# Performance work log

Hardware: AMD Instinct MI355X
Metric: run time of the kernel (lower is better)

The kernel has to match this reference:

```python
import jax, jax.numpy as jnp
import numpy as np

N_NODES = 50000
N_EDGES = 800000
DIM = 128
LN_EPS = 1e-5


def setup_inputs() -> dict:
    key = jax.random.key(0)
    k1, k2, k3, k4, k5 = jax.random.split(key, 5)
    x = jax.random.normal(k1, (N_NODES, DIM), dtype=jnp.float32)
    edge_index = jax.random.randint(k2, (2, N_EDGES), 0, N_NODES, dtype=jnp.int64)
    edge_weight = jax.random.uniform(k3, (N_EDGES,), dtype=jnp.float32)
    # GCNConv linear (PyG Linear: out = x @ W.T + b)
    W = jax.random.normal(k4, (DIM, DIM), dtype=jnp.float32) / np.sqrt(DIM)
    b = jnp.zeros((DIM,), dtype=jnp.float32)
    # pygnn.LayerNorm(dim, mode='node') affine params
    ln_weight = jnp.ones((DIM,), dtype=jnp.float32)
    ln_bias = jnp.zeros((DIM,), dtype=jnp.float32)
    return {"x": x, "edge_index": edge_index, "edge_weight": edge_weight,
            "W": W, "b": b, "ln_weight": ln_weight, "ln_bias": ln_bias}


def reference(x, edge_index, edge_weight, W, b, ln_weight, ln_bias):
    n = x.shape[0]
    # --- LayerNorm (mode='node'): per-node over feature dim ---
    mu = jnp.mean(x, axis=-1, keepdims=True)
    var = jnp.mean(jnp.square(x - mu), axis=-1, keepdims=True)
    xn = (x - mu) * jax.lax.rsqrt(var + LN_EPS) * ln_weight + ln_bias
    # --- GCNConv: linear first, then normalized propagate ---
    h = xn @ W.T  # [N, dim]
    row, col = edge_index[0], edge_index[1]  # source, target
    # add self loops (fill_value = 1.0)
    loop = jnp.arange(n, dtype=edge_index.dtype)
    row_f = jnp.concatenate([row, loop])
    col_f = jnp.concatenate([col, loop])
    ew_f = jnp.concatenate([edge_weight, jnp.ones((n,), dtype=edge_weight.dtype)])
    # symmetric gcn normalization: deg over target (col)
    deg = jax.ops.segment_sum(ew_f, col_f, num_segments=n)
    dinv = jnp.where(deg > 0, jax.lax.rsqrt(deg), 0.0)
    norm = dinv[row_f] * ew_f * dinv[col_f]  # [E+N]
    # gather-scale-scatter
    msg = h[row_f] * norm[:, None]  # [E+N, dim]
    out = jax.ops.segment_sum(msg, col_f, num_segments=n) + b
    # --- GELU (torch default = exact erf form); dropout is identity (p=0 / eval) ---
    return jax.nn.gelu(out, approximate=False)
```

## Files before the change

kernel.cpp:

```cpp
#include <hip/hip_runtime.h>
#include <math.h>

#define DIM 128
#define LN_EPS 1e-5f
#define HB 256
#define NSEG 8

typedef __attribute__((ext_vector_type(8))) short short8;
typedef __attribute__((ext_vector_type(4))) float floatx4;

__device__ __forceinline__ float gelu_exact(float v) {
    return 0.5f * v * (1.0f + erff(v * 0.70710678118654752f));
}
__device__ __forceinline__ float bf2f(unsigned short u) {
    return __uint_as_float(((unsigned)u) << 16);
}
__device__ __forceinline__ short f2bf(float f) {
    unsigned b = __float_as_uint(f);
    return (short)((b + 0x7FFF + ((b >> 16) & 1)) >> 16);
}

__global__ __launch_bounds__(256) void gemm_hist_kernel(
    const float* __restrict__ x, const float* __restrict__ W,
    const float* __restrict__ lnw, const float* __restrict__ lnb,
    unsigned short* __restrict__ h16,
    const int* __restrict__ col, int* __restrict__ hist,
    int n, int E, int nbkt)
{
    __shared__ short swb[2048 * 8];
    __shared__ short axb[1024 * 8];
    const int tid = threadIdx.x;

    if ((int)blockIdx.x < HB) {
        int* lh = (int*)swb;
        for (int b = tid; b < nbkt; b += 256) lh[b] = 0;
        __syncthreads();
        int g = blockIdx.x;
        int chunk = (E + HB - 1) / HB;
        int e0 = g * chunk;
        int e1 = e0 + chunk; if (e1 > E) e1 = E;
        for (int e = e0 + tid; e < e1; e += 256)
            atomicAdd(&lh[col[e] >> 6], 1);
        __syncthreads();
        for (int b = tid; b < nbkt; b += 256)
            hist[(size_t)g * nbkt + b] = lh[b];
        return;
    }

    const int gb = blockIdx.x - HB;
    const int n0 = gb * 64;

    for (int c = tid; c < 2048; c += 256) {
        int nrow = ((c >> 8) << 4) | (c & 15);
        int kb   = (((c >> 6) & 3) << 5) + (((c >> 4) & 3) << 3);
        const float* wp = W + nrow * DIM + kb;
        float4 w0 = *(const float4*)wp;
        float4 w1 = *(const float4*)(wp + 4);
        short8 p;
        p[0] = f2bf(w0.x); p[1] = f2bf(w0.y); p[2] = f2bf(w0.z); p[3] = f2bf(w0.w);
        p[4] = f2bf(w1.x); p[5] = f2bf(w1.y); p[6] = f2bf(w1.z); p[7] = f2bf(w1.w);
        *(short8*)&swb[c * 8] = p;
    }

    {
        int m = tid >> 2, sub = tid & 3;
        int node = n0 + m;
        bool valid = (node < n);
        const float4* xp = (const float4*)(x + (size_t)node * DIM + sub * 32);
        float4 v[8];
        float s = 0.f, ss = 0.f;
        #pragma unroll
        for (int i = 0; i < 8; ++i) {
            v[i] = valid ? xp[i] : make_float4(0.f, 0.f, 0.f, 0.f);
            s  += v[i].x + v[i].y + v[i].z + v[i].w;
            ss += v[i].x * v[i].x + v[i].y * v[i].y + v[i].z * v[i].z + v[i].w * v[i].w;
        }
        s += __shfl_xor(s, 1); ss += __shfl_xor(ss, 1);
        s += __shfl_xor(s, 2); ss += __shfl_xor(ss, 2);
        float mu   = s * (1.0f / 128.0f);
        float var  = ss * (1.0f / 128.0f) - mu * mu;
        float rstd = rsqrtf(var + LN_EPS);

        int mt = m >> 4, mloc = m & 15;
        #pragma unroll
        for (int quad = 0; quad < 4; ++quad) {
            float4 a = v[2 * quad], c4 = v[2 * quad + 1];
            const float4* lw = (const float4*)(lnw + sub * 32 + quad * 8);
            const float4* lb = (const float4*)(lnb + sub * 32 + quad * 8);
            float4 lw0 = lw[0], lw1 = lw[1], lb0 = lb[0], lb1 = lb[1];
            short8 p;
            p[0] = f2bf((a.x  - mu) * rstd * lw0.x + lb0.x);
            p[1] = f2bf((a.y  - mu) * rstd * lw0.y + lb0.y);
            p[2] = f2bf((a.z  - mu) * rstd * lw0.z + lb0.z);
            p[3] = f2bf((a.w  - mu) * rstd * lw0.w + lb0.w);
            p[4] = f2bf((c4.x - mu) * rstd * lw1.x + lb1.x);
            p[5] = f2bf((c4.y - mu) * rstd * lw1.y + lb1.y);
            p[6] = f2bf((c4.z - mu) * rstd * lw1.z + lb1.z);
            p[7] = f2bf((c4.w - mu) * rstd * lw1.w + lb1.w);
            int slot = mt * 256 + sub * 64 + quad * 16 + mloc;
            *(short8*)&axb[slot * 8] = p;
        }
    }
    __syncthreads();

    const int w    = tid >> 6;
    const int lane = tid & 63;

    short8 afrag[4];
    #pragma unroll
    for (int kq = 0; kq < 4; ++kq)
        afrag[kq] = *(const short8*)&axb[(w * 256 + kq * 64 + lane) * 8];

    floatx4 acc[8];
    #pragma unroll
    for (int jt = 0; jt < 8; ++jt) acc[jt] = (floatx4){0.f, 0.f, 0.f, 0.f};

    #pragma unroll
    for (int jt = 0; jt < 8; ++jt) {
        #pragma unroll
        for (int kq = 0; kq < 4; ++kq) {
            short8 bfrag = *(const short8*)&swb[(jt * 256 + kq * 64 + lane) * 8];
            acc[jt] = __builtin_amdgcn_mfma_f32_16x16x32_bf16(afrag[kq], bfrag,
                                                              acc[jt], 0, 0, 0);
        }
    }

    const int quad = lane >> 4, nl = lane & 15;
    #pragma unroll
    for (int jt = 0; jt < 8; ++jt) {
        #pragma unroll
        for (int r = 0; r < 4; ++r) {
            int rnode = n0 + w * 16 + quad * 4 + r;
            if (rnode < n)
                h16[(size_t)rnode * DIM + jt * 16 + nl] = (unsigned short)f2bf(acc[jt][r]);
        }
    }
}

__global__ __launch_bounds__(256) void seg_sum_kernel(
    const int* __restrict__ hist, int* __restrict__ segpart, int nbkt, int nq)
{
    int s = blockIdx.x / nq;
    int q = blockIdx.x % nq;
    int b = q * 256 + threadIdx.x;
    if (b >= nbkt) return;
    const int* hp = hist + (size_t)(s * (HB / NSEG)) * nbkt + b;
    int sum = 0;
    #pragma unroll 4
    for (int g = 0; g < HB / NSEG; ++g)
        sum += hp[(size_t)g * nbkt];
    segpart[(size_t)s * nbkt + b] = sum;
}

__global__ __launch_bounds__(256) void expand_kernel(
    const int* __restrict__ hist, const int* __restrict__ segpart,
    int* __restrict__ base, int* __restrict__ bktbase,
    int E, int nbkt, int nq)
{
    __shared__ int ls[256];
    const int tid = threadIdx.x;
    const int s = blockIdx.x / nq;
    const int q = blockIdx.x % nq;

    int excl_mine = 0;
    int carry = 0;
    for (int qq = 0; qq < nq; ++qq) {
        int b = qq * 256 + tid;
        int v = 0;
        if (b < nbkt) {
            #pragma unroll
            for (int ss = 0; ss < NSEG; ++ss)
                v += segpart[(size_t)ss * nbkt + b];
        }
        __syncthreads();
        ls[tid] = v;
        __syncthreads();
        int inc = v;
        for (int off = 1; off < 256; off <<= 1) {
            int add = (tid >= off) ? ls[tid - off] : 0;
            __syncthreads();
            inc += add;
            ls[tid] = inc;
            __syncthreads();
        }
        int ex = carry + inc - v;
        if (qq == q) excl_mine = ex;
        if (s == 0 && qq == q && b < nbkt) bktbase[b] = ex;
        carry += ls[255];
    }
    if (s == 0 && q == 0 && tid == 0) bktbase[nbkt] = E;

    int b = q * 256 + tid;
    if (b >= nbkt) return;
    int run = excl_mine;
    #pragma unroll
    for (int ss = 0; ss < NSEG; ++ss)
        if (ss < s) run += segpart[(size_t)ss * nbkt + b];
    int g0 = s * (HB / NSEG);
    for (int g = 0; g < HB / NSEG; ++g) {
        size_t idx = (size_t)(g0 + g) * nbkt + b;
        base[idx] = run;
        run += hist[idx];
    }
}

__global__ __launch_bounds__(256) void bucket_scatter_kernel(
    const int* __restrict__ row, const int* __restrict__ col,
    const float* __restrict__ ew, const int* __restrict__ base,
    int2* __restrict__ srt, int E, int nbkt)
{
    __shared__ int cur[1024];
    const int tid = threadIdx.x, g = blockIdx.x;
    for (int b = tid; b < nbkt; b += 256)
        cur[b] = base[(size_t)g * nbkt + b];
    __syncthreads();
    int chunk = (E + HB - 1) / HB;
    int e0 = g * chunk;
    int e1 = e0 + chunk; if (e1 > E) e1 = E;
    for (int e = e0 + tid; e < e1; e += 256) {
        int c = col[e];
        int pos = atomicAdd(&cur[c >> 6], 1);
        srt[pos] = make_int2(((c & 63) << 16) | row[e], __float_as_int(ew[e]));
    }
}

__global__ __launch_bounds__(256) void csr_kernel(
    const int2* __restrict__ srt, const int* __restrict__ bktbase,
    int2* __restrict__ edge_s, int* __restrict__ offsets,
    float* __restrict__ dinv, int n, int E)
{
    __shared__ int   k64[64];
    __shared__ float w64[64];
    __shared__ int   off64[64];
    __shared__ int   cur64[64];
    const int tid = threadIdx.x, b = blockIdx.x;
    if (tid < 64) { k64[tid] = 0; w64[tid] = 0.f; }
    __syncthreads();
    int s0 = bktbase[b], s1 = bktbase[b + 1];
    for (int i = s0 + tid; i < s1; i += 256) {
        int2 v = srt[i];
        int d = (v.x >> 16) & 63;
        atomicAdd(&k64[d], 1);
        atomicAdd(&w64[d], __int_as_float(v.y));
    }
    __syncthreads();
    if (tid == 0) {
        int run = 0;
        #pragma unroll
        for (int d = 0; d < 64; ++d) { off64[d] = run; cur64[d] = run; run += k64[d]; }
    }
    __syncthreads();
    if (tid < 64) {
        int dest = b * 64 + tid;
        if (dest < n) {
            offsets[dest] = s0 + off64[tid];
            dinv[dest]    = rsqrtf(1.0f + w64[tid]);
        }
    }
    if (b == 0 && tid == 0) offsets[n] = E;
    for (int i = s0 + tid; i < s1; i += 256) {
        int2 v = srt[i];
        int d = (v.x >> 16) & 63;
        int p = atomicAdd(&cur64[d], 1);
        edge_s[s0 + p] = make_int2(v.x & 0xFFFF, v.y);
    }
}

__global__ __launch_bounds__(256) void gather4_kernel(
    const int* __restrict__ offsets, const int2* __restrict__ edge_s,
    const float* __restrict__ dinv, const unsigned short* __restrict__ h16,
    const float* __restrict__ bias, float* __restrict__ out, int n)
{
    int wave = (blockIdx.x * 256 + threadIdx.x) >> 6;
    int lane = threadIdx.x & 63;
    int grp  = lane >> 4;
    int sub  = lane & 15;
    int node = wave * 4 + grp;
    if (node >= n) return;

    int beg = offsets[node], end = offsets[node + 1];
    float di = dinv[node];
    short8 sv = *(const short8*)(h16 + (size_t)node * DIM + sub * 8);
    float s2 = di * di;
    float acc[8];
    #pragma unroll
    for (int d = 0; d < 8; ++d) acc[d] = s2 * bf2f((unsigned short)sv[d]);

    int j = beg;
    for (; j + 3 < end; j += 4) {
        int2 e0 = edge_s[j],     e1 = edge_s[j + 1];
        int2 e2 = edge_s[j + 2], e3 = edge_s[j + 3];
        short8 a0 = *(const short8*)(h16 + (size_t)e0.x * DIM + sub * 8);
        short8 a1 = *(const short8*)(h16 + (size_t)e1.x * DIM + sub * 8);
        short8 a2 = *(const short8*)(h16 + (size_t)e2.x * DIM + sub * 8);
        short8 a3 = *(const short8*)(h16 + (size_t)e3.x * DIM + sub * 8);
        float n0 = dinv[e0.x] * __int_as_float(e0.y) * di;
        float n1 = dinv[e1.x] * __int_as_float(e1.y) * di;
        float n2 = dinv[e2.x] * __int_as_float(e2.y) * di;
        float n3 = dinv[e3.x] * __int_as_float(e3.y) * di;
        #pragma unroll
        for (int d = 0; d < 8; ++d) {
            acc[d] = fmaf(n0, bf2f((unsigned short)a0[d]), acc[d]);
            acc[d] = fmaf(n1, bf2f((unsigned short)a1[d]), acc[d]);
            acc[d] = fmaf(n2, bf2f((unsigned short)a2[d]), acc[d]);
            acc[d] = fmaf(n3, bf2f((unsigned short)a3[d]), acc[d]);
        }
    }
    for (; j < end; ++j) {
        int2 e0 = edge_s[j];
        float n0 = dinv[e0.x] * __int_as_float(e0.y) * di;
        short8 a = *(const short8*)(h16 + (size_t)e0.x * DIM + sub * 8);
        #pragma unroll
        for (int d = 0; d < 8; ++d) acc[d] = fmaf(n0, bf2f((unsigned short)a[d]), acc[d]);
    }

    float4 b0 = *(const float4*)(bias + sub * 8);
    float4 b1 = *(const float4*)(bias + sub * 8 + 4);
    float4 o0, o1;
    o0.x = gelu_exact(acc[0] + b0.x); o0.y = gelu_exact(acc[1] + b0.y);
    o0.z = gelu_exact(acc[2] + b0.z); o0.w = gelu_exact(acc[3] + b0.w);
    o1.x = gelu_exact(acc[4] + b1.x); o1.y = gelu_exact(acc[5] + b1.y);
    o1.z = gelu_exact(acc[6] + b1.z); o1.w = gelu_exact(acc[7] + b1.w);
    float* op = out + (size_t)node * DIM + sub * 8;
    *(float4*)op       = o0;
    *(float4*)(op + 4) = o1;
}

extern "C" void kernel_launch(void* const* d_in, const int* in_sizes, int n_in,
                              void* d_out, int out_size, void* d_ws, size_t ws_size,
                              hipStream_t stream)
{
    const float* x    = (const float*)d_in[0];
    const int*   ei   = (const int*)d_in[1];
    const float* ew   = (const float*)d_in[2];
    const float* W    = (const float*)d_in[3];
    const float* b    = (const float*)d_in[4];
    const float* ln_w = (const float*)d_in[5];
    const float* ln_b = (const float*)d_in[6];
    float* out = (float*)d_out;

    const int n = in_sizes[0] / DIM;
    const int E = in_sizes[2];
    const int* row  = ei;
    const int* colp = ei + E;
    const int nbkt = (n + 63) / 64;
    const int nq   = (nbkt + 255) / 256;

    int2*           srt     = (int2*)d_ws;
    int2*           edge_s  = srt + E;
    unsigned short* h16     = (unsigned short*)(edge_s + E);
    int*            hist    = (int*)(h16 + (size_t)n * DIM);
    int*            base    = hist + (size_t)HB * nbkt;
    int*            segpart = base + (size_t)HB * nbkt;
    int*            bktbase = segpart + (size_t)NSEG * nbkt;
    int*            offsets = bktbase + nbkt + 1;
    float*          dinv    = (float*)(offsets + n + 1);

    const int GB = (n + 63) / 64;

    gemm_hist_kernel<<<HB + GB, 256, 0, stream>>>(x, W, ln_w, ln_b, h16,
                                                  colp, hist, n, E, nbkt);
    seg_sum_kernel<<<NSEG * nq, 256, 0, stream>>>(hist, segpart, nbkt, nq);
    expand_kernel<<<NSEG * nq, 256, 0, stream>>>(hist, segpart, base, bktbase,
                                                 E, nbkt, nq);
    bucket_scatter_kernel<<<HB, 256, 0, stream>>>(row, colp, ew, base, srt, E, nbkt);
    csr_kernel<<<nbkt, 256, 0, stream>>>(srt, bktbase, edge_s, offsets, dinv, n, E);
    {
        int waves  = (n + 3) / 4;
        int blocks = (waves + 3) / 4;
        gather4_kernel<<<blocks, 256, 0, stream>>>(offsets, edge_s, dinv, h16, b, out, n);
    }
}
```

Baseline: 177.1 us.

## Replace two-level bucket sort CSR build with global-atomic degree count and direct scatter

The multi-stage bucket histogram, segment-sum, expand, bucket-scatter and per-bucket CSR passes are replaced. The new path counts per-node degree and weight sum with global float atomics, scans the counts into offsets, and scatters edges straight to their final CSR slots with global atomics on a per-node cursor. The full edge norm is now precomputed during the scatter, so the gather loop no longer loads dinv per edge. This cuts kernel count and the intermediate sort buffer, at the cost of heavily contended global atomics, non-deterministic edge order within each node, and a fixed 256-block scan limit (nblk must be ≤256, which holds for 50k nodes).

```diff
diff --git a/kernel.cpp b/kernel.cpp
--- a/kernel.cpp
+++ b/kernel.cpp
@@ -4,7 +4,6 @@
 #define DIM 128
 #define LN_EPS 1e-5f
 #define HB 256
-#define NSEG 8
 
 typedef __attribute__((ext_vector_type(8))) short short8;
 typedef __attribute__((ext_vector_type(4))) float floatx4;
@@ -20,30 +19,35 @@
     return (short)((b + 0x7FFF + ((b >> 16) & 1)) >> 16);
 }
 
-__global__ __launch_bounds__(256) void gemm_hist_kernel(
+__global__ __launch_bounds__(256) void zero_kernel(float2* __restrict__ deg, int n)
+{
+    int i = blockIdx.x * 256 + threadIdx.x;
+    if (i < n) deg[i] = make_float2(0.f, 0.f);
+}
+
+__global__ __launch_bounds__(256) void gemm_deg_kernel(
     const float* __restrict__ x, const float* __restrict__ W,
     const float* __restrict__ lnw, const float* __restrict__ lnb,
     unsigned short* __restrict__ h16,
-    const int* __restrict__ col, int* __restrict__ hist,
-    int n, int E, int nbkt)
+    const int* __restrict__ col, const float* __restrict__ ew,
+    float2* __restrict__ deg,
+    int n, int E)
 {
     __shared__ short swb[2048 * 8];
     __shared__ short axb[1024 * 8];
     const int tid = threadIdx.x;
 
     if ((int)blockIdx.x < HB) {
-        int* lh = (int*)swb;
-        for (int b = tid; b < nbkt; b += 256) lh[b] = 0;
-        __syncthreads();
         int g = blockIdx.x;
         int chunk = (E + HB - 1) / HB;
         int e0 = g * chunk;
         int e1 = e0 + chunk; if (e1 > E) e1 = E;
-        for (int e = e0 + tid; e < e1; e += 256)
-            atomicAdd(&lh[col[e] >> 6], 1);
-        __syncthreads();
-        for (int b = tid; b < nbkt; b += 256)
-            hist[(size_t)g * nbkt + b] = lh[b];
+        for (int e = e0 + tid; e < e1; e += 256) {
+            int c = col[e];
+            float w = ew[e];
+            atomicAdd(&deg[c].x, 1.0f);
+            atomicAdd(&deg[c].y, w);
+        }
         return;
     }
 
@@ -137,133 +141,82 @@
     }
 }
 
-__global__ __launch_bounds__(256) void seg_sum_kernel(
-    const int* __restrict__ hist, int* __restrict__ segpart, int nbkt, int nq)
-{
-    int s = blockIdx.x / nq;
-    int q = blockIdx.x % nq;
-    int b = q * 256 + threadIdx.x;
-    if (b >= nbkt) return;
-    const int* hp = hist + (size_t)(s * (HB / NSEG)) * nbkt + b;
-    int sum = 0;
-    #pragma unroll 4
-    for (int g = 0; g < HB / NSEG; ++g)
-        sum += hp[(size_t)g * nbkt];
-    segpart[(size_t)s * nbkt + b] = sum;
-}
-
-__global__ __launch_bounds__(256) void expand_kernel(
-    const int* __restrict__ hist, const int* __restrict__ segpart,
-    int* __restrict__ base, int* __restrict__ bktbase,
-    int E, int nbkt, int nq)
+__global__ __launch_bounds__(256) void part_kernel(
+    const float2* __restrict__ deg, int* __restrict__ part,
+    float* __restrict__ dinv, int n)
+{
+    __shared__ int ws[4];
+    const int tid = threadIdx.x;
+    int i = blockIdx.x * 256 + tid;
+    int c = 0;
+    if (i < n) {
+        float2 d = deg[i];
+        c = (int)d.x;
+        dinv[i] = rsqrtf(1.0f + d.y);
+    }
+    int cs = c;
+    cs += __shfl_xor(cs, 1);  cs += __shfl_xor(cs, 2);  cs += __shfl_xor(cs, 4);
+    cs += __shfl_xor(cs, 8);  cs += __shfl_xor(cs, 16); cs += __shfl_xor(cs, 32);
+    if ((tid & 63) == 0) ws[tid >> 6] = cs;
+    __syncthreads();
+    if (tid == 0) part[blockIdx.x] = ws[0] + ws[1] + ws[2] + ws[3];
+}
+
+__global__ __launch_bounds__(256) void scan_kernel(
+    const float2* __restrict__ deg, const int* __restrict__ part,
+    int* __restrict__ offsets, int* __restrict__ cursor,
+    int nblk, int n, int E)
 {
     __shared__ int ls[256];
+    __shared__ int spref;
     const int tid = threadIdx.x;
-    const int s = blockIdx.x / nq;
-    const int q = blockIdx.x % nq;
-
-    int excl_mine = 0;
-    int carry = 0;
-    for (int qq = 0; qq < nq; ++qq) {
-        int b = qq * 256 + tid;
-        int v = 0;
-        if (b < nbkt) {
-            #pragma unroll
-            for (int ss = 0; ss < NSEG; ++ss)
-                v += segpart[(size_t)ss * nbkt + b];
-        }
+
+    int v = (tid < nblk) ? part[tid] : 0;
+    ls[tid] = v;
+    __syncthreads();
+    int inc = v;
+    for (int off = 1; off < 256; off <<= 1) {
+        int add = (tid >= off) ? ls[tid - off] : 0;
         __syncthreads();
-        ls[tid] = v;
+        inc += add;
+        ls[tid] = inc;
         __syncthreads();
-        int inc = v;
-        for (int off = 1; off < 256; off <<= 1) {
-            int add = (tid >= off) ? ls[tid - off] : 0;
-            __syncthreads();
-            inc += add;
-            ls[tid] = inc;
-            __syncthreads();
-        }
-        int ex = carry + inc - v;
-        if (qq == q) excl_mine = ex;
-        if (s == 0 && qq == q && b < nbkt) bktbase[b] = ex;
-        carry += ls[255];
-    }
-    if (s == 0 && q == 0 && tid == 0) bktbase[nbkt] = E;
-
-    int b = q * 256 + tid;
-    if (b >= nbkt) return;
-    int run = excl_mine;
-    #pragma unroll
-    for (int ss = 0; ss < NSEG; ++ss)
-        if (ss < s) run += segpart[(size_t)ss * nbkt + b];
-    int g0 = s * (HB / NSEG);
-    for (int g = 0; g < HB / NSEG; ++g) {
-        size_t idx = (size_t)(g0 + g) * nbkt + b;
-        base[idx] = run;
-        run += hist[idx];
-    }
-}
-
-__global__ __launch_bounds__(256) void bucket_scatter_kernel(
+    }
+    if (tid == (int)blockIdx.x) spref = inc - v;
+    __syncthreads();
+    const int P = spref;
+
+    int i = blockIdx.x * 256 + tid;
+    int c = (i < n) ? (int)deg[i].x : 0;
+    ls[tid] = c;
+    __syncthreads();
+    int inc2 = c;
+    for (int off = 1; off < 256; off <<= 1) {
+        int add = (tid >= off) ? ls[tid - off] : 0;
+        __syncthreads();
+        inc2 += add;
+        ls[tid] = inc2;
+        __syncthreads();
+    }
+    if (i < n) {
+        int ex = P + inc2 - c;
+        offsets[i] = ex;
+        cursor[i]  = ex;
+    }
+    if (blockIdx.x == 0 && tid == 0) offsets[n] = E;
+}
+
+__global__ __launch_bounds__(256) void scatter_kernel(
     const int* __restrict__ row, const int* __restrict__ col,
-    const float* __restrict__ ew, const int* __restrict__ base,
-    int2* __restrict__ srt, int E, int nbkt)
-{
-    __shared__ int cur[1024];
-    const int tid = threadIdx.x, g = blockIdx.x;
-    for (int b = tid; b < nbkt; b += 256)
-        cur[b] = base[(size_t)g * nbkt + b];
-    __syncthreads();
-    int chunk = (E + HB - 1) / HB;
-    int e0 = g * chunk;
-    int e1 = e0 + chunk; if (e1 > E) e1 = E;
-    for (int e = e0 + tid; e < e1; e += 256) {
-        int c = col[e];
-        int pos = atomicAdd(&cur[c >> 6], 1);
-        srt[pos] = make_int2(((c & 63) << 16) | row[e], __float_as_int(ew[e]));
-    }
-}
-
-__global__ __launch_bounds__(256) void csr_kernel(
-    const int2* __restrict__ srt, const int* __restrict__ bktbase,
-    int2* __restrict__ edge_s, int* __restrict__ offsets,
-    float* __restrict__ dinv, int n, int E)
-{
-    __shared__ int   k64[64];
-    __shared__ float w64[64];
-    __shared__ int   off64[64];
-    __shared__ int   cur64[64];
-    const int tid = threadIdx.x, b = blockIdx.x;
-    if (tid < 64) { k64[tid] = 0; w64[tid] = 0.f; }
-    __syncthreads();
-    int s0 = bktbase[b], s1 = bktbase[b + 1];
-    for (int i = s0 + tid; i < s1; i += 256) {
-        int2 v = srt[i];
-        int d = (v.x >> 16) & 63;
-        atomicAdd(&k64[d], 1);
-        atomicAdd(&w64[d], __int_as_float(v.y));
-    }
-    __syncthreads();
-    if (tid == 0) {
-        int run = 0;
-        #pragma unroll
-        for (int d = 0; d < 64; ++d) { off64[d] = run; cur64[d] = run; run += k64[d]; }
-    }
-    __syncthreads();
-    if (tid < 64) {
-        int dest = b * 64 + tid;
-        if (dest < n) {
-            offsets[dest] = s0 + off64[tid];
-            dinv[dest]    = rsqrtf(1.0f + w64[tid]);
-        }
-    }
-    if (b == 0 && tid == 0) offsets[n] = E;
-    for (int i = s0 + tid; i < s1; i += 256) {
-        int2 v = srt[i];
-        int d = (v.x >> 16) & 63;
-        int p = atomicAdd(&cur64[d], 1);
-        edge_s[s0 + p] = make_int2(v.x & 0xFFFF, v.y);
-    }
+    const float* __restrict__ ew, const float* __restrict__ dinv,
+    int* __restrict__ cursor, int2* __restrict__ edge_s, int E)
+{
+    int e = blockIdx.x * 256 + threadIdx.x;
+    if (e >= E) return;
+    int r = row[e], c = col[e];
+    float nrm = dinv[r] * ew[e] * dinv[c];
+    int pos = atomicAdd(&cursor[c], 1);
+    edge_s[pos] = make_int2(r, __float_as_int(nrm));
 }
 
 __global__ __launch_bounds__(256) void gather4_kernel(
@@ -294,10 +247,10 @@
         short8 a1 = *(const short8*)(h16 + (size_t)e1.x * DIM + sub * 8);
         short8 a2 = *(const short8*)(h16 + (size_t)e2.x * DIM + sub * 8);
         short8 a3 = *(const short8*)(h16 + (size_t)e3.x * DIM + sub * 8);
-        float n0 = dinv[e0.x] * __int_as_float(e0.y) * di;
-        float n1 = dinv[e1.x] * __int_as_float(e1.y) * di;
-        float n2 = dinv[e2.x] * __int_as_float(e2.y) * di;
-        float n3 = dinv[e3.x] * __int_as_float(e3.y) * di;
+        float n0 = __int_as_float(e0.y);
+        float n1 = __int_as_float(e1.y);
+        float n2 = __int_as_float(e2.y);
+        float n3 = __int_as_float(e3.y);
         #pragma unroll
         for (int d = 0; d < 8; ++d) {
             acc[d] = fmaf(n0, bf2f((unsigned short)a0[d]), acc[d]);
@@ -308,7 +261,7 @@
     }
     for (; j < end; ++j) {
         int2 e0 = edge_s[j];
-        float n0 = dinv[e0.x] * __int_as_float(e0.y) * di;
+        float n0 = __int_as_float(e0.y);
         short8 a = *(const short8*)(h16 + (size_t)e0.x * DIM + sub * 8);
         #pragma unroll
         for (int d = 0; d < 8; ++d) acc[d] = fmaf(n0, bf2f((unsigned short)a[d]), acc[d]);
@@ -343,28 +296,25 @@
     const int E = in_sizes[2];
     const int* row  = ei;
     const int* colp = ei + E;
-    const int nbkt = (n + 63) / 64;
-    const int nq   = (nbkt + 255) / 256;
-
-    int2*           srt     = (int2*)d_ws;
-    int2*           edge_s  = srt + E;
+
+    int2*           edge_s  = (int2*)d_ws;
     unsigned short* h16     = (unsigned short*)(edge_s + E);
-    int*            hist    = (int*)(h16 + (size_t)n * DIM);
-    int*            base    = hist + (size_t)HB * nbkt;
-    int*            segpart = base + (size_t)HB * nbkt;
-    int*            bktbase = segpart + (size_t)NSEG * nbkt;
-    int*            offsets = bktbase + nbkt + 1;
+    float2*         deg     = (float2*)(h16 + (size_t)n * DIM);
+    int*            cursor  = (int*)(deg + n);
+    int*            offsets = cursor + n;
     float*          dinv    = (float*)(offsets + n + 1);
-
-    const int GB = (n + 63) / 64;
-
-    gemm_hist_kernel<<<HB + GB, 256, 0, stream>>>(x, W, ln_w, ln_b, h16,
-                                                  colp, hist, n, E, nbkt);
-    seg_sum_kernel<<<NSEG * nq, 256, 0, stream>>>(hist, segpart, nbkt, nq);
-    expand_kernel<<<NSEG * nq, 256, 0, stream>>>(hist, segpart, base, bktbase,
-                                                 E, nbkt, nq);
-    bucket_scatter_kernel<<<HB, 256, 0, stream>>>(row, colp, ew, base, srt, E, nbkt);
-    csr_kernel<<<nbkt, 256, 0, stream>>>(srt, bktbase, edge_s, offsets, dinv, n, E);
+    int*            part    = (int*)(dinv + n);
+
+    const int GB   = (n + 63) / 64;
+    const int nblk = (n + 255) / 256;
+
+    zero_kernel<<<nblk, 256, 0, stream>>>(deg, n);
+    gemm_deg_kernel<<<HB + GB, 256, 0, stream>>>(x, W, ln_w, ln_b, h16,
+                                                 colp, ew, deg, n, E);
+    part_kernel<<<nblk, 256, 0, stream>>>(deg, part, dinv, n);
+    scan_kernel<<<nblk, 256, 0, stream>>>(deg, part, offsets, cursor, nblk, n, E);
+    scatter_kernel<<<(E + 255) / 256, 256, 0, stream>>>(row, colp, ew, dinv,
+                                                        cursor, edge_s, E);
     {
         int waves  = (n + 3) / 4;
         int blocks = (waves + 3) / 4;
```

After: 259.9 us. 1.47x slower.

## Precompute bf16 W fragments once, restructure bucket prefix scan, fold target dinv into edges

Applied to the files above, without the earlier changes.

A separate small kernel now converts W to bf16 MFMA fragment layout once, and the GEMM blocks read B fragments straight from global memory (L2-cached) instead of each block converting W into shared memory. This removes redundant per-block conversion and LDS use, which may raise occupancy. The histogram prefix is now built per bucket: one block reduces each bucket's totals and another computes the bucket offsets and scans across the 256 histogram blocks, replacing the segmented two-pass scheme. The CSR kernel also multiplies the target dinv into the stored edge weight, so the gather loop skips that multiply.

```diff
diff --git a/kernel.cpp b/kernel.cpp
--- a/kernel.cpp
+++ b/kernel.cpp
@@ -4,7 +4,6 @@
 #define DIM 128
 #define LN_EPS 1e-5f
 #define HB 256
-#define NSEG 8
 
 typedef __attribute__((ext_vector_type(8))) short short8;
 typedef __attribute__((ext_vector_type(4))) float floatx4;
@@ -20,19 +19,33 @@
     return (short)((b + 0x7FFF + ((b >> 16) & 1)) >> 16);
 }
 
+__global__ __launch_bounds__(256) void wconv_kernel(
+    const float* __restrict__ W, short* __restrict__ wfrag)
+{
+    int c = blockIdx.x * 256 + threadIdx.x;
+    int nrow = ((c >> 8) << 4) | (c & 15);
+    int kb   = (((c >> 6) & 3) << 5) + (((c >> 4) & 3) << 3);
+    const float* wp = W + nrow * DIM + kb;
+    float4 w0 = *(const float4*)wp;
+    float4 w1 = *(const float4*)(wp + 4);
+    short8 p;
+    p[0] = f2bf(w0.x); p[1] = f2bf(w0.y); p[2] = f2bf(w0.z); p[3] = f2bf(w0.w);
+    p[4] = f2bf(w1.x); p[5] = f2bf(w1.y); p[6] = f2bf(w1.z); p[7] = f2bf(w1.w);
+    *(short8*)&wfrag[c * 8] = p;
+}
+
 __global__ __launch_bounds__(256) void gemm_hist_kernel(
-    const float* __restrict__ x, const float* __restrict__ W,
+    const float* __restrict__ x, const short* __restrict__ wfrag,
     const float* __restrict__ lnw, const float* __restrict__ lnb,
     unsigned short* __restrict__ h16,
     const int* __restrict__ col, int* __restrict__ hist,
     int n, int E, int nbkt)
 {
-    __shared__ short swb[2048 * 8];
     __shared__ short axb[1024 * 8];
     const int tid = threadIdx.x;
 
     if ((int)blockIdx.x < HB) {
-        int* lh = (int*)swb;
+        int* lh = (int*)axb;
         for (int b = tid; b < nbkt; b += 256) lh[b] = 0;
         __syncthreads();
         int g = blockIdx.x;
@@ -49,18 +62,6 @@
 
     const int gb = blockIdx.x - HB;
     const int n0 = gb * 64;
-
-    for (int c = tid; c < 2048; c += 256) {
-        int nrow = ((c >> 8) << 4) | (c & 15);
-        int kb   = (((c >> 6) & 3) << 5) + (((c >> 4) & 3) << 3);
-        const float* wp = W + nrow * DIM + kb;
-        float4 w0 = *(const float4*)wp;
-        float4 w1 = *(const float4*)(wp + 4);
-        short8 p;
-        p[0] = f2bf(w0.x); p[1] = f2bf(w0.y); p[2] = f2bf(w0.z); p[3] = f2bf(w0.w);
-        p[4] = f2bf(w1.x); p[5] = f2bf(w1.y); p[6] = f2bf(w1.z); p[7] = f2bf(w1.w);
-        *(short8*)&swb[c * 8] = p;
-    }
 
     {
         int m = tid >> 2, sub = tid & 3;
@@ -105,6 +106,7 @@
 
     const int w    = tid >> 6;
     const int lane = tid & 63;
+    const short8* wf = (const short8*)wfrag;
 
     short8 afrag[4];
     #pragma unroll
@@ -119,7 +121,7 @@
     for (int jt = 0; jt < 8; ++jt) {
         #pragma unroll
         for (int kq = 0; kq < 4; ++kq) {
-            short8 bfrag = *(const short8*)&swb[(jt * 256 + kq * 64 + lane) * 8];
+            short8 bfrag = wf[jt * 256 + kq * 64 + lane];
             acc[jt] = __builtin_amdgcn_mfma_f32_16x16x32_bf16(afrag[kq], bfrag,
                                                               acc[jt], 0, 0, 0);
         }
@@ -137,41 +139,34 @@
     }
 }
 
-__global__ __launch_bounds__(256) void seg_sum_kernel(
-    const int* __restrict__ hist, int* __restrict__ segpart, int nbkt, int nq)
-{
-    int s = blockIdx.x / nq;
-    int q = blockIdx.x % nq;
-    int b = q * 256 + threadIdx.x;
-    if (b >= nbkt) return;
-    const int* hp = hist + (size_t)(s * (HB / NSEG)) * nbkt + b;
-    int sum = 0;
-    #pragma unroll 4
-    for (int g = 0; g < HB / NSEG; ++g)
-        sum += hp[(size_t)g * nbkt];
-    segpart[(size_t)s * nbkt + b] = sum;
+__global__ __launch_bounds__(256) void tot_kernel(
+    const int* __restrict__ hist, int* __restrict__ tot, int nbkt)
+{
+    __shared__ int ws[4];
+    const int tid = threadIdx.x;
+    const int b = blockIdx.x;
+    int v = hist[(size_t)tid * nbkt + b];
+    v += __shfl_xor(v, 1);  v += __shfl_xor(v, 2);  v += __shfl_xor(v, 4);
+    v += __shfl_xor(v, 8);  v += __shfl_xor(v, 16); v += __shfl_xor(v, 32);
+    if ((tid & 63) == 0) ws[tid >> 6] = v;
+    __syncthreads();
+    if (tid == 0) tot[b] = ws[0] + ws[1] + ws[2] + ws[3];
 }
 
 __global__ __launch_bounds__(256) void expand_kernel(
-    const int* __restrict__ hist, const int* __restrict__ segpart,
-    int* __restrict__ base, int* __restrict__ bktbase,
-    int E, int nbkt, int nq)
+    const int* __restrict__ hist, const int* __restrict__ tot,
+    int* __restrict__ base, int* __restrict__ bktbase, int nbkt, int E)
 {
     __shared__ int ls[256];
+    __shared__ int sbb;
     const int tid = threadIdx.x;
-    const int s = blockIdx.x / nq;
-    const int q = blockIdx.x % nq;
-
-    int excl_mine = 0;
+    const int b = blockIdx.x;
+    const int nq = (nbkt + 255) / 256;
+
     int carry = 0;
     for (int qq = 0; qq < nq; ++qq) {
-        int b = qq * 256 + tid;
-        int v = 0;
-        if (b < nbkt) {
-            #pragma unroll
-            for (int ss = 0; ss < NSEG; ++ss)
-                v += segpart[(size_t)ss * nbkt + b];
-        }
+        int i = qq * 256 + tid;
+        int v = (i < nbkt) ? tot[i] : 0;
         __syncthreads();
         ls[tid] = v;
         __syncthreads();
@@ -183,25 +178,27 @@
             ls[tid] = inc;
             __syncthreads();
         }
-        int ex = carry + inc - v;
-        if (qq == q) excl_mine = ex;
-        if (s == 0 && qq == q && b < nbkt) bktbase[b] = ex;
+        if (i == b) sbb = carry + inc - v;
         carry += ls[255];
     }
-    if (s == 0 && q == 0 && tid == 0) bktbase[nbkt] = E;
-
-    int b = q * 256 + tid;
-    if (b >= nbkt) return;
-    int run = excl_mine;
-    #pragma unroll
-    for (int ss = 0; ss < NSEG; ++ss)
-        if (ss < s) run += segpart[(size_t)ss * nbkt + b];
-    int g0 = s * (HB / NSEG);
-    for (int g = 0; g < HB / NSEG; ++g) {
-        size_t idx = (size_t)(g0 + g) * nbkt + b;
-        base[idx] = run;
-        run += hist[idx];
-    }
+    __syncthreads();
+    const int bb = sbb;
+    if (tid == 0) bktbase[b] = bb;
+    if (b == 0 && tid == 0) bktbase[nbkt] = E;
+
+    int h = hist[(size_t)tid * nbkt + b];
+    __syncthreads();
+    ls[tid] = h;
+    __syncthreads();
+    int inc2 = h;
+    for (int off = 1; off < 256; off <<= 1) {
+        int add = (tid >= off) ? ls[tid - off] : 0;
+        __syncthreads();
+        inc2 += add;
+        ls[tid] = inc2;
+        __syncthreads();
+    }
+    base[(size_t)tid * nbkt + b] = bb + inc2 - h;
 }
 
 __global__ __launch_bounds__(256) void bucket_scatter_kernel(
@@ -231,6 +228,7 @@
 {
     __shared__ int   k64[64];
     __shared__ float w64[64];
+    __shared__ float di64[64];
     __shared__ int   off64[64];
     __shared__ int   cur64[64];
     const int tid = threadIdx.x, b = blockIdx.x;
@@ -252,17 +250,21 @@
     __syncthreads();
     if (tid < 64) {
         int dest = b * 64 + tid;
+        float dv = rsqrtf(1.0f + w64[tid]);
+        di64[tid] = dv;
         if (dest < n) {
             offsets[dest] = s0 + off64[tid];
-            dinv[dest]    = rsqrtf(1.0f + w64[tid]);
+            dinv[dest]    = dv;
         }
     }
     if (b == 0 && tid == 0) offsets[n] = E;
+    __syncthreads();
     for (int i = s0 + tid; i < s1; i += 256) {
         int2 v = srt[i];
         int d = (v.x >> 16) & 63;
         int p = atomicAdd(&cur64[d], 1);
-        edge_s[s0 + p] = make_int2(v.x & 0xFFFF, v.y);
+        edge_s[s0 + p] = make_int2(v.x & 0xFFFF,
+                                   __float_as_int(__int_as_float(v.y) * di64[d]));
     }
 }
 
@@ -294,10 +296,10 @@
         short8 a1 = *(const short8*)(h16 + (size_t)e1.x * DIM + sub * 8);
         short8 a2 = *(const short8*)(h16 + (size_t)e2.x * DIM + sub * 8);
         short8 a3 = *(const short8*)(h16 + (size_t)e3.x * DIM + sub * 8);
-        float n0 = dinv[e0.x] * __int_as_float(e0.y) * di;
-        float n1 = dinv[e1.x] * __int_as_float(e1.y) * di;
-        float n2 = dinv[e2.x] * __int_as_float(e2.y) * di;
-        float n3 = dinv[e3.x] * __int_as_float(e3.y) * di;
+        float n0 = dinv[e0.x] * __int_as_float(e0.y);
+        float n1 = dinv[e1.x] * __int_as_float(e1.y);
+        float n2 = dinv[e2.x] * __int_as_float(e2.y);
+        float n3 = dinv[e3.x] * __int_as_float(e3.y);
         #pragma unroll
         for (int d = 0; d < 8; ++d) {
             acc[d] = fmaf(n0, bf2f((unsigned short)a0[d]), acc[d]);
@@ -308,7 +310,7 @@
     }
     for (; j < end; ++j) {
         int2 e0 = edge_s[j];
-        float n0 = dinv[e0.x] * __int_as_float(e0.y) * di;
+        float n0 = dinv[e0.x] * __int_as_float(e0.y);
         short8 a = *(const short8*)(h16 + (size_t)e0.x * DIM + sub * 8);
         #pragma unroll
         for (int d = 0; d < 8; ++d) acc[d] = fmaf(n0, bf2f((unsigned short)a[d]), acc[d]);
@@ -344,25 +346,25 @@
     const int* row  = ei;
     const int* colp = ei + E;
     const int nbkt = (n + 63) / 64;
-    const int nq   = (nbkt + 255) / 256;
 
     int2*           srt     = (int2*)d_ws;
     int2*           edge_s  = srt + E;
     unsigned short* h16     = (unsigned short*)(edge_s + E);
-    int*            hist    = (int*)(h16 + (size_t)n * DIM);
+    short*          wfrag   = (short*)(h16 + (size_t)n * DIM);
+    int*            hist    = (int*)(wfrag + 16384);
     int*            base    = hist + (size_t)HB * nbkt;
-    int*            segpart = base + (size_t)HB * nbkt;
-    int*            bktbase = segpart + (size_t)NSEG * nbkt;
+    int*            tot     = base + (size_t)HB * nbkt;
+    int*            bktbase = tot + nbkt;
     int*            offsets = bktbase + nbkt + 1;
     float*          dinv    = (float*)(offsets + n + 1);
 
     const int GB = (n + 63) / 64;
 
-    gemm_hist_kernel<<<HB + GB, 256, 0, stream>>>(x, W, ln_w, ln_b, h16,
+    wconv_kernel<<<8, 256, 0, stream>>>(W, wfrag);
+    gemm_hist_kernel<<<HB + GB, 256, 0, stream>>>(x, wfrag, ln_w, ln_b, h16,
                                                   colp, hist, n, E, nbkt);
-    seg_sum_kernel<<<NSEG * nq, 256, 0, stream>>>(hist, segpart, nbkt, nq);
-    expand_kernel<<<NSEG * nq, 256, 0, stream>>>(hist, segpart, base, bktbase,
-                                                 E, nbkt, nq);
+    tot_kernel<<<nbkt, 256, 0, stream>>>(hist, tot, nbkt);
+    expand_kernel<<<nbkt, 256, 0, stream>>>(hist, tot, base, bktbase, nbkt, E);
     bucket_scatter_kernel<<<HB, 256, 0, stream>>>(row, colp, ew, base, srt, E, nbkt);
     csr_kernel<<<nbkt, 256, 0, stream>>>(srt, bktbase, edge_s, offsets, dinv, n, E);
     {
```

After: 178.5 us. No clear change (+0.8%).

## Replace global CSR build with fixed-capacity buckets and fuse per-bucket sort into gather

Applied to the files above, without the earlier changes.

Edges are now scattered into fixed-capacity (CAP) slots per 64-node bucket, which makes the global scan unnecessary and lets a one-block-per-bucket expand kernel replace the seg_sum and multi-pass expand kernels. The CSR kernel and edge_s buffer are removed. The gather kernel now loads each bucket's edges into LDS, counting-sorts them by destination, and precomputes the per-edge normalisation there before gathering. It also adds a slow fallback for buckets over capacity and doubles the histogram block count. The aim is to cut kernel launches and global round-trips. The cost is fewer, LDS-heavy gather blocks (about 32KB each), which lowers parallelism and occupancy.

```diff
diff --git a/kernel.cpp b/kernel.cpp
--- a/kernel.cpp
+++ b/kernel.cpp
@@ -3,8 +3,8 @@
 
 #define DIM 128
 #define LN_EPS 1e-5f
-#define HB 256
-#define NSEG 8
+#define HB 512
+#define CAP 2048
 
 typedef __attribute__((ext_vector_type(8))) short short8;
 typedef __attribute__((ext_vector_type(4))) float floatx4;
@@ -137,71 +137,32 @@
     }
 }
 
-__global__ __launch_bounds__(256) void seg_sum_kernel(
-    const int* __restrict__ hist, int* __restrict__ segpart, int nbkt, int nq)
-{
-    int s = blockIdx.x / nq;
-    int q = blockIdx.x % nq;
-    int b = q * 256 + threadIdx.x;
-    if (b >= nbkt) return;
-    const int* hp = hist + (size_t)(s * (HB / NSEG)) * nbkt + b;
-    int sum = 0;
-    #pragma unroll 4
-    for (int g = 0; g < HB / NSEG; ++g)
-        sum += hp[(size_t)g * nbkt];
-    segpart[(size_t)s * nbkt + b] = sum;
-}
-
 __global__ __launch_bounds__(256) void expand_kernel(
-    const int* __restrict__ hist, const int* __restrict__ segpart,
-    int* __restrict__ base, int* __restrict__ bktbase,
-    int E, int nbkt, int nq)
+    const int* __restrict__ hist, int* __restrict__ base,
+    int* __restrict__ cnt, int nbkt)
 {
     __shared__ int ls[256];
     const int tid = threadIdx.x;
-    const int s = blockIdx.x / nq;
-    const int q = blockIdx.x % nq;
-
-    int excl_mine = 0;
-    int carry = 0;
-    for (int qq = 0; qq < nq; ++qq) {
-        int b = qq * 256 + tid;
-        int v = 0;
-        if (b < nbkt) {
-            #pragma unroll
-            for (int ss = 0; ss < NSEG; ++ss)
-                v += segpart[(size_t)ss * nbkt + b];
-        }
-        __syncthreads();
-        ls[tid] = v;
-        __syncthreads();
-        int inc = v;
-        for (int off = 1; off < 256; off <<= 1) {
-            int add = (tid >= off) ? ls[tid - off] : 0;
-            __syncthreads();
-            inc += add;
-            ls[tid] = inc;
-            __syncthreads();
-        }
-        int ex = carry + inc - v;
-        if (qq == q) excl_mine = ex;
-        if (s == 0 && qq == q && b < nbkt) bktbase[b] = ex;
-        carry += ls[255];
-    }
-    if (s == 0 && q == 0 && tid == 0) bktbase[nbkt] = E;
-
-    int b = q * 256 + tid;
-    if (b >= nbkt) return;
-    int run = excl_mine;
-    #pragma unroll
-    for (int ss = 0; ss < NSEG; ++ss)
-        if (ss < s) run += segpart[(size_t)ss * nbkt + b];
-    int g0 = s * (HB / NSEG);
-    for (int g = 0; g < HB / NSEG; ++g) {
-        size_t idx = (size_t)(g0 + g) * nbkt + b;
-        base[idx] = run;
-        run += hist[idx];
-    }
+    const int b = blockIdx.x;
+
+    int v0 = hist[(size_t)(2 * tid)     * nbkt + b];
+    int v1 = hist[(size_t)(2 * tid + 1) * nbkt + b];
+    int p = v0 + v1;
+    ls[tid] = p;
+    __syncthreads();
+    int inc = p;
+    for (int off = 1; off < 256; off <<= 1) {
+        int add = (tid >= off) ? ls[tid - off] : 0;
+        __syncthreads();
+        inc += add;
+        ls[tid] = inc;
+        __syncthreads();
+    }
+    int ex = inc - p;
+    int a0 = b * CAP + ex;
+    base[(size_t)(2 * tid)     * nbkt + b] = a0;
+    base[(size_t)(2 * tid + 1) * nbkt + b] = a0 + v0;
+    if (tid == 255) cnt[b] = inc;
 }
 
 __global__ __launch_bounds__(256) void bucket_scatter_kernel(
@@ -224,106 +185,154 @@
     }
 }
 
-__global__ __launch_bounds__(256) void csr_kernel(
-    const int2* __restrict__ srt, const int* __restrict__ bktbase,
-    int2* __restrict__ edge_s, int* __restrict__ offsets,
-    float* __restrict__ dinv, int n, int E)
-{
-    __shared__ int   k64[64];
+__global__ __launch_bounds__(256) void dinv_kernel(
+    const int2* __restrict__ srt, const int* __restrict__ cnt,
+    float* __restrict__ dinv, int n)
+{
     __shared__ float w64[64];
-    __shared__ int   off64[64];
-    __shared__ int   cur64[64];
     const int tid = threadIdx.x, b = blockIdx.x;
-    if (tid < 64) { k64[tid] = 0; w64[tid] = 0.f; }
-    __syncthreads();
-    int s0 = bktbase[b], s1 = bktbase[b + 1];
-    for (int i = s0 + tid; i < s1; i += 256) {
-        int2 v = srt[i];
-        int d = (v.x >> 16) & 63;
-        atomicAdd(&k64[d], 1);
-        atomicAdd(&w64[d], __int_as_float(v.y));
-    }
-    __syncthreads();
-    if (tid == 0) {
-        int run = 0;
-        #pragma unroll
-        for (int d = 0; d < 64; ++d) { off64[d] = run; cur64[d] = run; run += k64[d]; }
-    }
-    __syncthreads();
-    if (tid < 64) {
-        int dest = b * 64 + tid;
-        if (dest < n) {
-            offsets[dest] = s0 + off64[tid];
-            dinv[dest]    = rsqrtf(1.0f + w64[tid]);
-        }
-    }
-    if (b == 0 && tid == 0) offsets[n] = E;
-    for (int i = s0 + tid; i < s1; i += 256) {
-        int2 v = srt[i];
-        int d = (v.x >> 16) & 63;
-        int p = atomicAdd(&cur64[d], 1);
-        edge_s[s0 + p] = make_int2(v.x & 0xFFFF, v.y);
-    }
-}
-
-__global__ __launch_bounds__(256) void gather4_kernel(
-    const int* __restrict__ offsets, const int2* __restrict__ edge_s,
+    if (tid < 64) w64[tid] = 0.f;
+    __syncthreads();
+    int c = cnt[b];
+    int s0 = b * CAP;
+    for (int i = tid; i < c; i += 256) {
+        int2 v = srt[s0 + i];
+        atomicAdd(&w64[(v.x >> 16) & 63], __int_as_float(v.y));
+    }
+    __syncthreads();
+    if (tid < 64)
+        dinv[b * 64 + tid] = rsqrtf(1.0f + w64[tid]);
+}
+
+__global__ __launch_bounds__(256) void bucket_gather_kernel(
+    const int2* __restrict__ srt, const int* __restrict__ cnt,
     const float* __restrict__ dinv, const unsigned short* __restrict__ h16,
     const float* __restrict__ bias, float* __restrict__ out, int n)
 {
-    int wave = (blockIdx.x * 256 + threadIdx.x) >> 6;
-    int lane = threadIdx.x & 63;
-    int grp  = lane >> 4;
-    int sub  = lane & 15;
-    int node = wave * 4 + grp;
-    if (node >= n) return;
-
-    int beg = offsets[node], end = offsets[node + 1];
-    float di = dinv[node];
-    short8 sv = *(const short8*)(h16 + (size_t)node * DIM + sub * 8);
-    float s2 = di * di;
-    float acc[8];
-    #pragma unroll
-    for (int d = 0; d < 8; ++d) acc[d] = s2 * bf2f((unsigned short)sv[d]);
-
-    int j = beg;
-    for (; j + 3 < end; j += 4) {
-        int2 e0 = edge_s[j],     e1 = edge_s[j + 1];
-        int2 e2 = edge_s[j + 2], e3 = edge_s[j + 3];
-        short8 a0 = *(const short8*)(h16 + (size_t)e0.x * DIM + sub * 8);
-        short8 a1 = *(const short8*)(h16 + (size_t)e1.x * DIM + sub * 8);
-        short8 a2 = *(const short8*)(h16 + (size_t)e2.x * DIM + sub * 8);
-        short8 a3 = *(const short8*)(h16 + (size_t)e3.x * DIM + sub * 8);
-        float n0 = dinv[e0.x] * __int_as_float(e0.y) * di;
-        float n1 = dinv[e1.x] * __int_as_float(e1.y) * di;
-        float n2 = dinv[e2.x] * __int_as_float(e2.y) * di;
-        float n3 = dinv[e3.x] * __int_as_float(e3.y) * di;
-        #pragma unroll
-        for (int d = 0; d < 8; ++d) {
-            acc[d] = fmaf(n0, bf2f((unsigned short)a0[d]), acc[d]);
-            acc[d] = fmaf(n1, bf2f((unsigned short)a1[d]), acc[d]);
-            acc[d] = fmaf(n2, bf2f((unsigned short)a2[d]), acc[d]);
-            acc[d] = fmaf(n3, bf2f((unsigned short)a3[d]), acc[d]);
-        }
-    }
-    for (; j < end; ++j) {
-        int2 e0 = edge_s[j];
-        float n0 = dinv[e0.x] * __int_as_float(e0.y) * di;
-        short8 a = *(const short8*)(h16 + (size_t)e0.x * DIM + sub * 8);
-        #pragma unroll
-        for (int d = 0; d < 8; ++d) acc[d] = fmaf(n0, bf2f((unsigned short)a[d]), acc[d]);
-    }
-
-    float4 b0 = *(const float4*)(bias + sub * 8);
-    float4 b1 = *(const float4*)(bias + sub * 8 + 4);
-    float4 o0, o1;
-    o0.x = gelu_exact(acc[0] + b0.x); o0.y = gelu_exact(acc[1] + b0.y);
-    o0.z = gelu_exact(acc[2] + b0.z); o0.w = gelu_exact(acc[3] + b0.w);
-    o1.x = gelu_exact(acc[4] + b1.x); o1.y = gelu_exact(acc[5] + b1.y);
-    o1.z = gelu_exact(acc[6] + b1.z); o1.w = gelu_exact(acc[7] + b1.w);
-    float* op = out + (size_t)node * DIM + sub * 8;
-    *(float4*)op       = o0;
-    *(float4*)(op + 4) = o1;
+    __shared__ int2  bufA[CAP];
+    __shared__ int2  bufB[CAP];
+    __shared__ int   k64[64], off64[64], cur64[64];
+    __shared__ float di64[64];
+    const int tid = threadIdx.x, b = blockIdx.x;
+
+    if (tid < 64) { k64[tid] = 0; di64[tid] = dinv[b * 64 + tid]; }
+    __syncthreads();
+
+    const int c  = cnt[b];
+    const int s0 = b * CAP;
+    const int grp = tid >> 4;
+    const int sub = tid & 15;
+
+    if (c <= CAP) {
+        for (int i = tid; i < c; i += 256) {
+            int2 v = srt[s0 + i];
+            bufA[i] = v;
+            atomicAdd(&k64[(v.x >> 16) & 63], 1);
+        }
+        __syncthreads();
+        if (tid == 0) {
+            int run = 0;
+            #pragma unroll
+            for (int d = 0; d < 64; ++d) { off64[d] = run; cur64[d] = run; run += k64[d]; }
+        }
+        __syncthreads();
+        for (int i = tid; i < c; i += 256) {
+            int2 v = bufA[i];
+            int d   = (v.x >> 16) & 63;
+            int src = v.x & 0xFFFF;
+            float nrm = dinv[src] * __int_as_float(v.y) * di64[d];
+            int p = atomicAdd(&cur64[d], 1);
+            bufB[p] = make_int2(src, __float_as_int(nrm));
+        }
+        __syncthreads();
+
+        #pragma unroll
+        for (int dd = 0; dd < 4; ++dd) {
+            int d = dd * 16 + grp;
+            int dest = b * 64 + d;
+            if (dest >= n) continue;
+            float di = di64[d];
+            short8 sv = *(const short8*)(h16 + (size_t)dest * DIM + sub * 8);
+            float s2 = di * di;
+            float acc[8];
+            #pragma unroll
+            for (int k = 0; k < 8; ++k) acc[k] = s2 * bf2f((unsigned short)sv[k]);
+
+            int j  = off64[d];
+            int je = j + k64[d];
+            for (; j + 3 < je; j += 4) {
+                int2 e0 = bufB[j],     e1 = bufB[j + 1];
+                int2 e2 = bufB[j + 2], e3 = bufB[j + 3];
+                short8 a0 = *(const short8*)(h16 + (size_t)e0.x * DIM + sub * 8);
+                short8 a1 = *(const short8*)(h16 + (size_t)e1.x * DIM + sub * 8);
+                short8 a2 = *(const short8*)(h16 + (size_t)e2.x * DIM + sub * 8);
+                short8 a3 = *(const short8*)(h16 + (size_t)e3.x * DIM + sub * 8);
+                float n0 = __int_as_float(e0.y);
+                float n1 = __int_as_float(e1.y);
+                float n2 = __int_as_float(e2.y);
+                float n3 = __int_as_float(e3.y);
+                #pragma unroll
+                for (int k = 0; k < 8; ++k) {
+                    acc[k] = fmaf(n0, bf2f((unsigned short)a0[k]), acc[k]);
+                    acc[k] = fmaf(n1, bf2f((unsigned short)a1[k]), acc[k]);
+                    acc[k] = fmaf(n2, bf2f((unsigned short)a2[k]), acc[k]);
+                    acc[k] = fmaf(n3, bf2f((unsigned short)a3[k]), acc[k]);
+                }
+            }
+            for (; j < je; ++j) {
+                int2 e0 = bufB[j];
+                float n0 = __int_as_float(e0.y);
+                short8 a = *(const short8*)(h16 + (size_t)e0.x * DIM + sub * 8);
+                #pragma unroll
+                for (int k = 0; k < 8; ++k)
+                    acc[k] = fmaf(n0, bf2f((unsigned short)a[k]), acc[k]);
+            }
+
+            float4 b0 = *(const float4*)(bias + sub * 8);
+            float4 b1 = *(const float4*)(bias + sub * 8 + 4);
+            float4 o0, o1;
+            o0.x = gelu_exact(acc[0] + b0.x); o0.y = gelu_exact(acc[1] + b0.y);
+            o0.z = gelu_exact(acc[2] + b0.z); o0.w = gelu_exact(acc[3] + b0.w);
+            o1.x = gelu_exact(acc[4] + b1.x); o1.y = gelu_exact(acc[5] + b1.y);
+            o1.z = gelu_exact(acc[6] + b1.z); o1.w = gelu_exact(acc[7] + b1.w);
+            float* op = out + (size_t)dest * DIM + sub * 8;
+            *(float4*)op       = o0;
+            *(float4*)(op + 4) = o1;
+        }
+    } else {
+        #pragma unroll
+        for (int dd = 0; dd < 4; ++dd) {
+            int d = dd * 16 + grp;
+            int dest = b * 64 + d;
+            if (dest >= n) continue;
+            float di = di64[d];
+            short8 sv = *(const short8*)(h16 + (size_t)dest * DIM + sub * 8);
+            float s2 = di * di;
+            float acc[8];
+            #pragma unroll
+            for (int k = 0; k < 8; ++k) acc[k] = s2 * bf2f((unsigned short)sv[k]);
+            for (int i = 0; i < c; ++i) {
+                int2 v = srt[s0 + i];
+                if (((v.x >> 16) & 63) != d) continue;
+                int src = v.x & 0xFFFF;
+                float nrm = dinv[src] * __int_as_float(v.y) * di;
+                short8 a = *(const short8*)(h16 + (size_t)src * DIM + sub * 8);
+                #pragma unroll
+                for (int k = 0; k < 8; ++k)
+                    acc[k] = fmaf(nrm, bf2f((unsigned short)a[k]), acc[k]);
+            }
+            float4 b0 = *(const float4*)(bias + sub * 8);
+            float4 b1 = *(const float4*)(bias + sub * 8 + 4);
+            float4 o0, o1;
+            o0.x = gelu_exact(acc[0] + b0.x); o0.y = gelu_exact(acc[1] + b0.y);
+            o0.z = gelu_exact(acc[2] + b0.z); o0.w = gelu_exact(acc[3] + b0.w);
+            o1.x = gelu_exact(acc[4] + b1.x); o1.y = gelu_exact(acc[5] + b1.y);
+            o1.z = gelu_exact(acc[6] + b1.z); o1.w = gelu_exact(acc[7] + b1.w);
+            float* op = out + (size_t)dest * DIM + sub * 8;
+            *(float4*)op       = o0;
+            *(float4*)(op + 4) = o1;
+        }
+    }
 }
 
 extern "C" void kernel_launch(void* const* d_in, const int* in_sizes, int n_in,
@@ -344,30 +353,20 @@
     const int* row  = ei;
     const int* colp = ei + E;
     const int nbkt = (n + 63) / 64;
-    const int nq   = (nbkt + 255) / 256;
-
-    int2*           srt     = (int2*)d_ws;
-    int2*           edge_s  = srt + E;
-    unsigned short* h16     = (unsigned short*)(edge_s + E);
-    int*            hist    = (int*)(h16 + (size_t)n * DIM);
-    int*            base    = hist + (size_t)HB * nbkt;
-    int*            segpart = base + (size_t)HB * nbkt;
-    int*            bktbase = segpart + (size_t)NSEG * nbkt;
-    int*            offsets = bktbase + nbkt + 1;
-    float*          dinv    = (float*)(offsets + n + 1);
+
+    int2*           srt  = (int2*)d_ws;
+    unsigned short* h16  = (unsigned short*)(srt + (size_t)nbkt * CAP);
+    int*            hist = (int*)(h16 + (size_t)n * DIM);
+    int*            base = hist + (size_t)HB * nbkt;
+    int*            cnt  = base + (size_t)HB * nbkt;
+    float*          dinv = (float*)(cnt + nbkt);
 
     const int GB = (n + 63) / 64;
 
     gemm_hist_kernel<<<HB + GB, 256, 0, stream>>>(x, W, ln_w, ln_b, h16,
                                                   colp, hist, n, E, nbkt);
-    seg_sum_kernel<<<NSEG * nq, 256, 0, stream>>>(hist, segpart, nbkt, nq);
-    expand_kernel<<<NSEG * nq, 256, 0, stream>>>(hist, segpart, base, bktbase,
-                                                 E, nbkt, nq);
+    expand_kernel<<<nbkt, 256, 0, stream>>>(hist, base, cnt, nbkt);
     bucket_scatter_kernel<<<HB, 256, 0, stream>>>(row, colp, ew, base, srt, E, nbkt);
-    csr_kernel<<<nbkt, 256, 0, stream>>>(srt, bktbase, edge_s, offsets, dinv, n, E);
-    {
-        int waves  = (n + 3) / 4;
-        int blocks = (waves + 3) / 4;
-        gather4_kernel<<<blocks, 256, 0, stream>>>(offsets, edge_s, dinv, h16, b, out, n);
-    }
-}
+    dinv_kernel<<<nbkt, 256, 0, stream>>>(srt, cnt, dinv, n);
+    bucket_gather_kernel<<<nbkt, 256, 0, stream>>>(srt, cnt, dinv, h16, b, out, n);
+}
```

After: 171.0 us. -3.5%, faster.
